# Kernel tuning notes

Hardware: AMD Instinct MI355X
Metric: run time of the kernel (lower is better)

Reference implementation:

```python
import jax, jax.numpy as jnp
import numpy as np

B, L, NB = 8192, 40, 2        # batch, maxlen, behavior features
V, E = 100000, 64             # vocab per table, embed dim per table
NS, ND = 3, 8                 # other sparse feats, dense feats
D = NB * E                    # concatenated behavior embed dim = 128
ALL = D + D + (ND + NS * E)   # info_all dim = 456
NEG_INF = -2.0**32 + 1
BN_EPS = 1e-3                 # keras BatchNormalization default epsilon


def setup_inputs() -> dict:
    key = jax.random.key(0)
    ks = jax.random.split(key, 20)
    inp = {
        "dense_inputs": jax.random.normal(ks[0], (B, ND), jnp.float32),
        "sparse_inputs": jax.random.randint(ks[1], (B, NS), 0, V),
        "seq_inputs": jax.random.randint(ks[2], (B, L, NB), 0, V),
        "item_inputs": jax.random.randint(ks[3], (B, NB), 0, V),
        # embedding tables (random_uniform init in keras)
        "emb_sparse": jax.random.uniform(ks[4], (NS, V, E), jnp.float32, -0.05, 0.05),
        "emb_seq": jax.random.uniform(ks[5], (NB, V, E), jnp.float32, -0.05, 0.05),
        # attention MLP: input 4*D=512 -> 80 -> 40 -> 1
        "att_W1": jax.random.normal(ks[6], (4 * D, 80), jnp.float32) * 0.05,
        "att_b1": jnp.zeros((80,), jnp.float32),
        "att_W2": jax.random.normal(ks[7], (80, 40), jnp.float32) * 0.05,
        "att_b2": jnp.zeros((40,), jnp.float32),
        "att_Wf": jax.random.normal(ks[8], (40, 1), jnp.float32) * 0.05,
        "att_bf": jnp.zeros((1,), jnp.float32),
        # batch norm (inference-mode moving stats)
        "bn_gamma": jnp.ones((ALL,), jnp.float32),
        "bn_beta": jnp.zeros((ALL,), jnp.float32),
        "bn_mean": jnp.zeros((ALL,), jnp.float32),
        "bn_var": jnp.ones((ALL,), jnp.float32),
        # FFN: ALL -> 80 -> 40 -> 1, PReLU alphas per-feature
        "ffn_W1": jax.random.normal(ks[9], (ALL, 80), jnp.float32) * 0.05,
        "ffn_b1": jnp.zeros((80,), jnp.float32),
        "ffn_a1": jnp.full((80,), 0.25, jnp.float32),
        "ffn_W2": jax.random.normal(ks[10], (80, 40), jnp.float32) * 0.05,
        "ffn_b2": jnp.zeros((40,), jnp.float32),
        "ffn_a2": jnp.full((40,), 0.25, jnp.float32),
        "out_W": jax.random.normal(ks[11], (40, 1), jnp.float32) * 0.05,
        "out_b": jnp.zeros((1,), jnp.float32),
    }
    return inp


def prelu(x, alpha):
    return jnp.where(x > 0, x, alpha * x)


def reference(dense_inputs, sparse_inputs, seq_inputs, item_inputs,
              emb_sparse, emb_seq,
              att_W1, att_b1, att_W2, att_b2, att_Wf, att_bf,
              bn_gamma, bn_beta, bn_mean, bn_var,
              ffn_W1, ffn_b1, ffn_a1, ffn_W2, ffn_b2, ffn_a2,
              out_W, out_b):
    mask = (seq_inputs[:, :, 0] != 0)                                   # [B, L]
    # other sparse embeddings + dense features
    other_info = jnp.concatenate(
        [dense_inputs] + [emb_sparse[i][sparse_inputs[:, i]] for i in range(NS)], axis=-1)
    # behavior sequence / candidate item embeddings
    seq_embed = jnp.concatenate([emb_seq[i][seq_inputs[:, :, i]] for i in range(NB)], axis=-1)  # [B,L,D]
    item_embed = jnp.concatenate([emb_seq[i][item_inputs[:, i]] for i in range(NB)], axis=-1)   # [B,D]

    # local activation attention
    q = jnp.broadcast_to(item_embed[:, None, :], seq_embed.shape)       # [B,L,D]
    info = jnp.concatenate([q, seq_embed, q - seq_embed, q * seq_embed], axis=-1)  # [B,L,4D]
    h = jax.nn.sigmoid(info @ att_W1 + att_b1)
    h = jax.nn.sigmoid(h @ att_W2 + att_b2)
    logits = (h @ att_Wf + att_bf)[..., 0]                               # [B,L]
    logits = jnp.where(mask, logits, NEG_INF)
    att = jax.nn.softmax(logits, axis=-1)                                # [B,L]
    user_info = jnp.einsum('bl,bld->bd', att, seq_embed)                 # [B,D]

    info_all = jnp.concatenate([user_info, item_embed, other_info], axis=-1)  # [B,ALL]
    info_all = bn_gamma * (info_all - bn_mean) * jax.lax.rsqrt(bn_var + BN_EPS) + bn_beta
    info_all = prelu(info_all @ ffn_W1 + ffn_b1, ffn_a1)
    info_all = prelu(info_all @ ffn_W2 + ffn_b2, ffn_a2)
    return jax.nn.sigmoid(info_all @ out_W + out_b)                      # [B,1]
```

## Files before the change

### kernel.cpp

```cpp
#include <hip/hip_runtime.h>

#define BB 8192
#define LL 40
#define VV 100000
#define NEG_INF_F (-4294967295.0f)
#define XS 136
#define HS 104
#define XGS 480

typedef __attribute__((ext_vector_type(8))) short short8;
typedef __attribute__((ext_vector_type(4))) float f32x4;

__device__ __forceinline__ unsigned cvt_pk_bf16(float a, float b) {
  unsigned r;
  asm("v_cvt_pk_bf16_f32 %0, %1, %2" : "=v"(r) : "v"(a), "v"(b));
  return r;
}
__device__ __forceinline__ unsigned short f2bf(float f) {
  return (unsigned short)cvt_pk_bf16(f, f);
}
__device__ __forceinline__ float bf2f(unsigned short s) {
  return __uint_as_float(((unsigned)s) << 16);
}
__device__ __forceinline__ float sigm(float z) {
  return __builtin_amdgcn_rcpf(1.f + __expf(-z));
}

__device__ __forceinline__ short8 fuseB(short8 wsd, short8 wd, float4 qa, float4 qb) {
  float qv[8] = {qa.x, qa.y, qa.z, qa.w, qb.x, qb.y, qb.z, qb.w};
  float f[8];
#pragma unroll
  for (int j = 0; j < 8; j++)
    f[j] = bf2f((unsigned short)wsd[j]) + qv[j] * bf2f((unsigned short)wd[j]);
  uint4 o;
  o.x = cvt_pk_bf16(f[0], f[1]);
  o.y = cvt_pk_bf16(f[2], f[3]);
  o.z = cvt_pk_bf16(f[4], f[5]);
  o.w = cvt_pk_bf16(f[6], f[7]);
  return __builtin_bit_cast(short8, o);
}

__global__ void prep_all(const float* __restrict__ W1, float* __restrict__ wqcT,
                         unsigned short* __restrict__ WsdpT,
                         const float* __restrict__ aW2, unsigned short* __restrict__ W2bT,
                         const float* __restrict__ fW2, unsigned short* __restrict__ W2fT,
                         const float* __restrict__ fW1, const float* __restrict__ g,
                         const float* __restrict__ vr, unsigned short* __restrict__ W1fT,
                         const float* __restrict__ fb1, const float* __restrict__ be,
                         const float* __restrict__ mn, float* __restrict__ b1p,
                         const float* __restrict__ embQ, unsigned short* __restrict__ embQb) {
  __shared__ float red[4];
  int bid = blockIdx.x, t = threadIdx.x;
  if (bid < 40) {
    int i = bid * 256 + t;
    int h = i >> 7, k = i & 127;
    float a = W1[k * 80 + h];
    float b = W1[(128 + k) * 80 + h];
    float c = W1[(256 + k) * 80 + h];
    float d = W1[(384 + k) * 80 + h];
    wqcT[h * 132 + k] = a + c;
    WsdpT[h * 256 + k] = f2bf(b - c);
    WsdpT[h * 256 + 128 + k] = f2bf(d);
  } else if (bid < 58) {
    int i = (bid - 40) * 256 + t;
    int n = i / 96, k = i % 96;
    W2bT[i] = (n < 40 && k < 80) ? f2bf(aW2[k * 40 + n]) : (unsigned short)0;
  } else if (bid < 76) {
    int i = (bid - 58) * 256 + t;
    int n = i / 96, k = i % 96;
    W2fT[i] = (n < 40 && k < 80) ? f2bf(fW2[k * 40 + n]) : (unsigned short)0;
  } else if (bid < 226) {
    int i = (bid - 76) * 256 + t;
    int n = i / 480, k = i % 480;
    float v = 0.f;
    if (k < 456) v = fW1[k * 80 + n] * g[k] * rsqrtf(vr[k] + 1e-3f);
    W1fT[i] = f2bf(v);
  } else if (bid < 306) {
    int n = bid - 226;
    float p = 0.f;
    for (int k = t; k < 456; k += 256) {
      float sc = g[k] * rsqrtf(vr[k] + 1e-3f);
      p += (be[k] - mn[k] * sc) * fW1[k * 80 + n];
    }
    for (int off = 32; off; off >>= 1) p += __shfl_xor(p, off, 64);
    if ((t & 63) == 0) red[t >> 6] = p;
    __syncthreads();
    if (t == 0) b1p[n] = fb1[n] + red[0] + red[1] + red[2] + red[3];
  } else {
    const float4* src = (const float4*)embQ;
    uint2* dst = (uint2*)embQb;
    for (int i = (bid - 306) * 256 + t; i < 3200000; i += 2048 * 256) {
      float4 v = src[i];
      uint2 p;
      p.x = cvt_pk_bf16(v.x, v.y);
      p.y = cvt_pk_bf16(v.z, v.w);
      dst[i] = p;
    }
  }
}


__launch_bounds__(256, 8)
__global__ void din_att(const float* __restrict__ dense, const int* __restrict__ sparsei,
                        const int* __restrict__ seqi, const int* __restrict__ itemi,
                        const float* __restrict__ embS, const float* __restrict__ embQ,
                        const unsigned short* __restrict__ embQb,
                        const float* __restrict__ wqcT, const unsigned short* __restrict__ WsdpT,
                        const unsigned short* __restrict__ W2bT,
                        const float* __restrict__ ab1, const float* __restrict__ ab2,
                        const float* __restrict__ aWf, const float* __restrict__ abf,
                        unsigned short* __restrict__ Xg) {
  __shared__ __align__(16) char smem[20352];
  unsigned short* sX  = (unsigned short*)smem;
  unsigned short* sH1 = (unsigned short*)(smem + 10880);
  float* sQ    = (float*)(smem + 19200);
  float* sQCp  = sQ + 128;
  float* sLA   = sQCp + 80;
  float* sMask = sLA + 40;

  const int t = threadIdx.x;
  const int b = blockIdx.x;
  const int wv = t >> 6, ln = t & 63, m16 = ln & 15, quad = ln >> 4;
  unsigned short* xrow = Xg + (size_t)b * XGS;

  if (t < 32) {
    int f = t >> 4, sub = t & 15;
    int idx = itemi[b * 2 + f];
    float4 v = *(const float4*)(embQ + ((size_t)(f * VV + idx)) * 64 + sub * 4);
    *(float4*)(sQ + f * 64 + sub * 4) = v;
    uint2 p;
    p.x = cvt_pk_bf16(v.x, v.y);
    p.y = cvt_pk_bf16(v.z, v.w);
    *(uint2*)(xrow + 128 + f * 64 + sub * 4) = p;
  } else if (t >= 100 && t < 140) {
    sLA[t - 100] = 0.f;
  }
  for (int i = t; i < 320; i += 256) {
    int r = i >> 3, c = i & 7;
    ((unsigned*)sH1)[r * 52 + 40 + c] = 0u;
  }
  __syncthreads();

  uint2 gv[5];
#pragma unroll
  for (int it = 0; it < 5; it++) {
    int i = t + (it << 8);
    int r = i >> 4, sub = i & 15, f = r & 1;
    int idx = seqi[b * 80 + r];
    if (embQb) {
      gv[it] = *(const uint2*)(embQb + ((size_t)(f * VV + idx)) * 64 + sub * 4);
    } else {
      float4 v = *(const float4*)(embQ + ((size_t)(f * VV + idx)) * 64 + sub * 4);
      gv[it].x = cvt_pk_bf16(v.x, v.y);
      gv[it].y = cvt_pk_bf16(v.z, v.w);
    }
  }
  if (t >= 32 && t < 80) {
    int j = t - 32, f = j >> 4, sub = j & 15;
    int idx = sparsei[b * 3 + f];
    float4 v = *(const float4*)(embS + ((size_t)(f * VV + idx)) * 64 + sub * 4);
    uint2 p;
    p.x = cvt_pk_bf16(v.x, v.y);
    p.y = cvt_pk_bf16(v.z, v.w);
    *(uint2*)(xrow + 264 + f * 64 + sub * 4) = p;
  } else if (t >= 80 && t < 88) {
    xrow[256 + (t - 80)] = f2bf(dense[b * 8 + (t - 80)]);
  } else if (t >= 88 && t < 100) {
    ((unsigned*)xrow)[228 + (t - 88)] = 0u;
  }
  if (t < 80) {
    float acc0 = ab1[t], acc1 = 0.f;
    const float* wq = wqcT + t * 132;
    for (int k = 0; k < 128; k += 8) {
      float4 w0 = *(const float4*)(wq + k);
      float4 w1 = *(const float4*)(wq + k + 4);
      float4 q0 = *(const float4*)(sQ + k);
      float4 q1 = *(const float4*)(sQ + k + 4);
      acc0 += q0.x * w0.x + q0.y * w0.y + q0.z * w0.z + q0.w * w0.w;
      acc1 += q1.x * w1.x + q1.y * w1.y + q1.z * w1.z + q1.w * w1.w;
    }
    sQCp[t] = acc0 + acc1;
  }
  short8 Bp[4];
  {
    const unsigned short* br = WsdpT + (size_t)(wv * 16 + m16) * 256 + quad * 8;
#pragma unroll
    for (int kt = 0; kt < 4; kt++) {
      short8 w1 = *(const short8*)(br + kt * 32);
      short8 w2 = *(const short8*)(br + 128 + kt * 32);
      int k0 = quad * 8 + kt * 32;
      Bp[kt] = fuseB(w1, w2, *(const float4*)(sQ + k0), *(const float4*)(sQ + k0 + 4));
    }
  }
#pragma unroll
  for (int it = 0; it < 5; it++) {
    int i = t + (it << 8);
    int r = i >> 4, sub = i & 15, l = r >> 1, f = r & 1;
    *(uint2*)(sX + l * XS + f * 64 + sub * 4) = gv[it];
  }
  if ((t & 31) == 0) {
#pragma unroll
    for (int it = 0; it < 5; it++) {
      int r = (t >> 4) + (it << 4);
      sMask[r >> 1] = (seqi[b * 80 + r] != 0) ? 0.f : NEG_INF_F;
    }
  }
  __syncthreads();

  {
    const int h = wv * 16 + m16;
    const float qc = sQCp[h];
#pragma unroll
    for (int mt = 0; mt < 3; mt++) {
      f32x4 acc = {0.f, 0.f, 0.f, 0.f};
      const unsigned short* ar = sX + (mt * 16 + m16) * XS + quad * 8;
#pragma unroll
      for (int kt = 0; kt < 4; kt++) {
        short8 a = *(const short8*)(ar + kt * 32);
        acc = __builtin_amdgcn_mfma_f32_16x16x32_bf16(a, Bp[kt], acc, 0, 0, 0);
      }
      float s0 = sigm(acc[0] + qc), s1 = sigm(acc[1] + qc);
      float s2 = sigm(acc[2] + qc), s3 = sigm(acc[3] + qc);
      unsigned p01 = cvt_pk_bf16(s0, s1), p23 = cvt_pk_bf16(s2, s3);
      int l0 = mt * 16 + quad * 4;
      if (l0 < 40) {
        sH1[(l0 + 0) * HS + h] = (unsigned short)p01;
        sH1[(l0 + 1) * HS + h] = (unsigned short)(p01 >> 16);
        sH1[(l0 + 2) * HS + h] = (unsigned short)p23;
        sH1[(l0 + 3) * HS + h] = (unsigned short)(p23 >> 16);
      }
    }
    if (wv < 3) {
      const unsigned short* br = WsdpT + (size_t)(64 + m16) * 256 + quad * 8;
      const unsigned short* ar = sX + (wv * 16 + m16) * XS + quad * 8;
      f32x4 acc = {0.f, 0.f, 0.f, 0.f};
#pragma unroll
      for (int kt = 0; kt < 4; kt++) {
        short8 w1 = *(const short8*)(br + kt * 32);
        short8 w2 = *(const short8*)(br + 128 + kt * 32);
        int k0 = quad * 8 + kt * 32;
        short8 bp = fuseB(w1, w2, *(const float4*)(sQ + k0), *(const float4*)(sQ + k0 + 4));
        short8 a = *(const short8*)(ar + kt * 32);
        acc = __builtin_amdgcn_mfma_f32_16x16x32_bf16(a, bp, acc, 0, 0, 0);
      }
      int h4 = 64 + m16;
      float qc4 = sQCp[h4];
      float s0 = sigm(acc[0] + qc4), s1 = sigm(acc[1] + qc4);
      float s2 = sigm(acc[2] + qc4), s3 = sigm(acc[3] + qc4);
      unsigned p01 = cvt_pk_bf16(s0, s1), p23 = cvt_pk_bf16(s2, s3);
      int l0 = wv * 16 + quad * 4;
      if (l0 < 40) {
        sH1[(l0 + 0) * HS + h4] = (unsigned short)p01;
        sH1[(l0 + 1) * HS + h4] = (unsigned short)(p01 >> 16);
        sH1[(l0 + 2) * HS + h4] = (unsigned short)p23;
        sH1[(l0 + 3) * HS + h4] = (unsigned short)(p23 >> 16);
      }
    }
  }
  __syncthreads();

  for (int tile = wv; tile < 9; tile += 4) {
    int mt = tile / 3, nt = tile % 3;
    f32x4 acc = {0.f, 0.f, 0.f, 0.f};
    int arow = mt * 16 + m16;
    if (arow > 39) arow = 39;
    const unsigned short* ar = sH1 + arow * HS + quad * 8;
    const unsigned short* br = W2bT + (nt * 16 + m16) * 96 + quad * 8;
#pragma unroll
    for (int kt = 0; kt < 3; kt++) {
      short8 a = *(const short8*)(ar + kt * 32);
      short8 bb = *(const short8*)(br + kt * 32);
      acc = __builtin_amdgcn_mfma_f32_16x16x32_bf16(a, bb, acc, 0, 0, 0);
    }
    int j = nt * 16 + m16;
    float b2 = (j < 40) ? ab2[j] : 0.f;
    float wf = (j < 40) ? aWf[j] : 0.f;
    float c[4];
#pragma unroll
    for (int r = 0; r < 4; r++) {
      float h2 = sigm(acc[r] + b2);
      c[r] = (j < 40) ? h2 * wf : 0.f;
    }
#pragma unroll
    for (int off = 1; off < 16; off <<= 1) {
#pragma unroll
      for (int r = 0; r < 4; r++) c[r] += __shfl_xor(c[r], off, 64);
    }
    if (m16 == 0) {
#pragma unroll
      for (int r = 0; r < 4; r++) {
        int l = mt * 16 + quad * 4 + r;
        if (l < 40) atomicAdd(&sLA[l], c[r]);
      }
    }
  }
  __syncthreads();

  if (wv < 2) {
    float logit = -3.0e38f;
    if (ln < 40) logit = sLA[ln] + abf[0] + sMask[ln];
    float mx = logit;
    for (int off = 32; off; off >>= 1) mx = fmaxf(mx, __shfl_xor(mx, off, 64));
    float ex = (ln < 40) ? __expf(logit - mx) : 0.f;
    float sm = ex;
    for (int off = 32; off; off >>= 1) sm += __shfl_xor(sm, off, 64);
    float* av = sQCp + wv * 40;
    if (ln < 40) av[ln] = ex * __builtin_amdgcn_rcpf(sm);
    float acc = 0.f;
    for (int l = 0; l < 40; l++) acc += av[l] * bf2f(sX[l * XS + t]);
    xrow[t] = f2bf(acc);
  }
}


__launch_bounds__(256, 2)
__global__ void din_ffn(const unsigned short* __restrict__ Xg,
                        const unsigned short* __restrict__ W1fT, const float* __restrict__ b1p,
                        const float* __restrict__ fa1,
                        const unsigned short* __restrict__ W2fT, const float* __restrict__ fb2,
                        const float* __restrict__ fa2,
                        const float* __restrict__ oW, const float* __restrict__ ob,
                        float* __restrict__ out) {
  __shared__ __align__(16) unsigned short sXB[16 * 488];
  __shared__ __align__(16) unsigned short sH1B[16 * HS];
  __shared__ float sH2B[16 * 41];
  const int t = threadIdx.x, blk = blockIdx.x;
  const int wv = t >> 6, ln = t & 63, m16 = ln & 15, quad = ln >> 4;

  short8 Bf[15];
  {
    const unsigned short* br = W1fT + (size_t)(wv * 16 + m16) * 480 + quad * 8;
#pragma unroll
    for (int kt = 0; kt < 15; kt++) Bf[kt] = *(const short8*)(br + kt * 32);
  }

  for (int i = t; i < 960; i += 256) {
    int r = i / 60, c = i % 60;
    *(uint4*)(sXB + r * 488 + c * 8) =
        *(const uint4*)(Xg + (size_t)(blk * 16 + r) * XGS + c * 8);
  }
  if (t < 128) {
    int r = t >> 3, c = t & 7;
    ((unsigned*)sH1B)[r * 52 + 40 + c] = 0u;
  }
  __syncthreads();

  {
    int h = wv * 16 + m16;
    f32x4 acc = {0.f, 0.f, 0.f, 0.f};
    const unsigned short* ar = sXB + m16 * 488 + quad * 8;
#pragma unroll
    for (int kt = 0; kt < 15; kt++) {
      short8 a = *(const short8*)(ar + kt * 32);
      acc = __builtin_amdgcn_mfma_f32_16x16x32_bf16(a, Bf[kt], acc, 0, 0, 0);
    }
    float b1v = b1p[h], a1v = fa1[h];
    float z0 = acc[0] + b1v, z1 = acc[1] + b1v, z2 = acc[2] + b1v, z3 = acc[3] + b1v;
    z0 = z0 > 0.f ? z0 : a1v * z0;
    z1 = z1 > 0.f ? z1 : a1v * z1;
    z2 = z2 > 0.f ? z2 : a1v * z2;
    z3 = z3 > 0.f ? z3 : a1v * z3;
    unsigned p01 = cvt_pk_bf16(z0, z1), p23 = cvt_pk_bf16(z2, z3);
    int l0 = quad * 4;
    sH1B[(l0 + 0) * HS + h] = (unsigned short)p01;
    sH1B[(l0 + 1) * HS + h] = (unsigned short)(p01 >> 16);
    sH1B[(l0 + 2) * HS + h] = (unsigned short)p23;
    sH1B[(l0 + 3) * HS + h] = (unsigned short)(p23 >> 16);
    if (wv == 0) {
      short8 B4[15];
      const unsigned short* br = W1fT + (size_t)(64 + m16) * 480 + quad * 8;
#pragma unroll
      for (int kt = 0; kt < 15; kt++) B4[kt] = *(const short8*)(br + kt * 32);
      f32x4 acc4 = {0.f, 0.f, 0.f, 0.f};
#pragma unroll
      for (int kt = 0; kt < 15; kt++) {
        short8 a = *(const short8*)(ar + kt * 32);
        acc4 = __builtin_amdgcn_mfma_f32_16x16x32_bf16(a, B4[kt], acc4, 0, 0, 0);
      }
      int h4 = 64 + m16;
      float b1v4 = b1p[h4], a1v4 = fa1[h4];
      float y0 = acc4[0] + b1v4, y1 = acc4[1] + b1v4, y2 = acc4[2] + b1v4, y3 = acc4[3] + b1v4;
      y0 = y0 > 0.f ? y0 : a1v4 * y0;
      y1 = y1 > 0.f ? y1 : a1v4 * y1;
      y2 = y2 > 0.f ? y2 : a1v4 * y2;
      y3 = y3 > 0.f ? y3 : a1v4 * y3;
      unsigned q01 = cvt_pk_bf16(y0, y1), q23 = cvt_pk_bf16(y2, y3);
      sH1B[(l0 + 0) * HS + h4] = (unsigned short)q01;
      sH1B[(l0 + 1) * HS + h4] = (unsigned short)(q01 >> 16);
      sH1B[(l0 + 2) * HS + h4] = (unsigned short)q23;
      sH1B[(l0 + 3) * HS + h4] = (unsigned short)(q23 >> 16);
    }
  }
  __syncthreads();

  if (wv < 3) {
    f32x4 acc = {0.f, 0.f, 0.f, 0.f};
    const unsigned short* ar = sH1B + m16 * HS + quad * 8;
    const unsigned short* br = W2fT + (wv * 16 + m16) * 96 + quad * 8;
#pragma unroll
    for (int kt = 0; kt < 3; kt++) {
      short8 a = *(const short8*)(ar + kt * 32);
      short8 bb = *(const short8*)(br + kt * 32);
      acc = __builtin_amdgcn_mfma_f32_16x16x32_bf16(a, bb, acc, 0, 0, 0);
    }
    int j = wv * 16 + m16;
    if (j < 40) {
      float b2 = fb2[j], a2 = fa2[j];
#pragma unroll
      for (int r = 0; r < 4; r++) {
        int l = quad * 4 + r;
        float z = acc[r] + b2;
        sH2B[l * 41 + j] = z > 0.f ? z : a2 * z;
      }
    }
  }
  __syncthreads();

  if (t < 16) {
    float acc = ob[0];
    for (int j = 0; j < 40; j++) acc += sH2B[t * 41 + j] * oW[j];
    out[blk * 16 + t] = sigm(acc);
  }
}


extern "C" void kernel_launch(void* const* d_in, const int* in_sizes, int n_in,
                              void* d_out, int out_size, void* d_ws, size_t ws_size,
                              hipStream_t stream) {
  const float* dense  = (const float*)d_in[0];
  const int*   sparsei = (const int*)d_in[1];
  const int*   seqi   = (const int*)d_in[2];
  const int*   itemi  = (const int*)d_in[3];
  const float* embS   = (const float*)d_in[4];
  const float* embQ   = (const float*)d_in[5];
  const float* aW1    = (const float*)d_in[6];
  const float* ab1    = (const float*)d_in[7];
  const float* aW2    = (const float*)d_in[8];
  const float* ab2    = (const float*)d_in[9];
  const float* aWf    = (const float*)d_in[10];
  const float* abf    = (const float*)d_in[11];
  const float* bng    = (const float*)d_in[12];
  const float* bnb    = (const float*)d_in[13];
  const float* bnm    = (const float*)d_in[14];
  const float* bnv    = (const float*)d_in[15];
  const float* fW1    = (const float*)d_in[16];
  const float* fb1    = (const float*)d_in[17];
  const float* fa1    = (const float*)d_in[18];
  const float* fW2    = (const float*)d_in[19];
  const float* fb2    = (const float*)d_in[20];
  const float* fa2    = (const float*)d_in[21];
  const float* oW     = (const float*)d_in[22];
  const float* ob     = (const float*)d_in[23];
  float* out = (float*)d_out;

  float* ws = (float*)d_ws;
  float* wqcT = ws;
  float* b1p  = ws + 10560;
  unsigned short* WsdpT = (unsigned short*)(ws + 10640);
  unsigned short* W2bT  = (unsigned short*)(ws + 20880);
  unsigned short* W2fT  = (unsigned short*)(ws + 23184);
  unsigned short* W1fT  = (unsigned short*)(ws + 25488);
  unsigned short* Xg    = (unsigned short*)(ws + 44688);

  size_t base = 44688ull * 4 + 8192ull * 480 * 2;
  size_t need = base + 12800000ull * 2;
  unsigned short* embQb = (ws_size >= need)
      ? (unsigned short*)((char*)d_ws + base) : (unsigned short*)0;

  int prep_grid = embQb ? 2354 : 306;
  prep_all<<<prep_grid, 256, 0, stream>>>(aW1, wqcT, WsdpT, aW2, W2bT, fW2, W2fT,
                                          fW1, bng, bnv, W1fT, fb1, bnb, bnm, b1p,
                                          embQ, embQb);
  din_att<<<BB, 256, 0, stream>>>(dense, sparsei, seqi, itemi, embS, embQ, embQb,
                                  wqcT, WsdpT, W2bT, ab1, ab2, aWf, abf, Xg);
  din_ffn<<<512, 256, 0, stream>>>(Xg, W1fT, b1p, fa1, W2fT, fb2, fa2, oW, ob, out);
}
```

Measured before the change: 335.5 us.

## Drop full bf16 table conversion; widen FFN block to five waves

Removes the prep pass that converted the entire 2x100000x64 fp32 sequence embedding table to bf16 on every call, and has the attention kernel gather fp32 rows directly and convert them in registers. This avoids reading about 51 MB and writing about 26 MB per call, at the cost of doubling the bytes fetched per gathered row. The FFN kernel is launched with 320 threads so a fifth wave computes the last 16 hidden units instead of wave 0 doing two tiles serially, and launch bounds and load strides are adjusted to match.

```diff
diff --git a/kernel.cpp b/kernel.cpp
--- a/kernel.cpp
+++ b/kernel.cpp
@@ -47,8 +47,7 @@
                          const float* __restrict__ fW1, const float* __restrict__ g,
                          const float* __restrict__ vr, unsigned short* __restrict__ W1fT,
                          const float* __restrict__ fb1, const float* __restrict__ be,
-                         const float* __restrict__ mn, float* __restrict__ b1p,
-                         const float* __restrict__ embQ, unsigned short* __restrict__ embQb) {
+                         const float* __restrict__ mn, float* __restrict__ b1p) {
   __shared__ float red[4];
   int bid = blockIdx.x, t = threadIdx.x;
   if (bid < 40) {
@@ -75,7 +74,7 @@
     float v = 0.f;
     if (k < 456) v = fW1[k * 80 + n] * g[k] * rsqrtf(vr[k] + 1e-3f);
     W1fT[i] = f2bf(v);
-  } else if (bid < 306) {
+  } else {
     int n = bid - 226;
     float p = 0.f;
     for (int k = t; k < 456; k += 256) {
@@ -86,16 +85,6 @@
     if ((t & 63) == 0) red[t >> 6] = p;
     __syncthreads();
     if (t == 0) b1p[n] = fb1[n] + red[0] + red[1] + red[2] + red[3];
-  } else {
-    const float4* src = (const float4*)embQ;
-    uint2* dst = (uint2*)embQb;
-    for (int i = (bid - 306) * 256 + t; i < 3200000; i += 2048 * 256) {
-      float4 v = src[i];
-      uint2 p;
-      p.x = cvt_pk_bf16(v.x, v.y);
-      p.y = cvt_pk_bf16(v.z, v.w);
-      dst[i] = p;
-    }
   }
 }
 
@@ -104,7 +93,6 @@
 __global__ void din_att(const float* __restrict__ dense, const int* __restrict__ sparsei,
                         const int* __restrict__ seqi, const int* __restrict__ itemi,
                         const float* __restrict__ embS, const float* __restrict__ embQ,
-                        const unsigned short* __restrict__ embQb,
                         const float* __restrict__ wqcT, const unsigned short* __restrict__ WsdpT,
                         const unsigned short* __restrict__ W2bT,
                         const float* __restrict__ ab1, const float* __restrict__ ab2,
@@ -147,13 +135,9 @@
     int i = t + (it << 8);
     int r = i >> 4, sub = i & 15, f = r & 1;
     int idx = seqi[b * 80 + r];
-    if (embQb) {
-      gv[it] = *(const uint2*)(embQb + ((size_t)(f * VV + idx)) * 64 + sub * 4);
-    } else {
-      float4 v = *(const float4*)(embQ + ((size_t)(f * VV + idx)) * 64 + sub * 4);
-      gv[it].x = cvt_pk_bf16(v.x, v.y);
-      gv[it].y = cvt_pk_bf16(v.z, v.w);
-    }
+    float4 v = *(const float4*)(embQ + ((size_t)(f * VV + idx)) * 64 + sub * 4);
+    gv[it].x = cvt_pk_bf16(v.x, v.y);
+    gv[it].y = cvt_pk_bf16(v.z, v.w);
   }
   if (t >= 32 && t < 80) {
     int j = t - 32, f = j >> 4, sub = j & 15;
@@ -313,7 +297,7 @@
 }
 
 
-__launch_bounds__(256, 2)
+__launch_bounds__(320, 2)
 __global__ void din_ffn(const unsigned short* __restrict__ Xg,
                         const unsigned short* __restrict__ W1fT, const float* __restrict__ b1p,
                         const float* __restrict__ fa1,
@@ -334,7 +318,7 @@
     for (int kt = 0; kt < 15; kt++) Bf[kt] = *(const short8*)(br + kt * 32);
   }
 
-  for (int i = t; i < 960; i += 256) {
+  for (int i = t; i < 960; i += 320) {
     int r = i / 60, c = i % 60;
     *(uint4*)(sXB + r * 488 + c * 8) =
         *(const uint4*)(Xg + (size_t)(blk * 16 + r) * XGS + c * 8);
@@ -366,30 +350,6 @@
     sH1B[(l0 + 1) * HS + h] = (unsigned short)(p01 >> 16);
     sH1B[(l0 + 2) * HS + h] = (unsigned short)p23;
     sH1B[(l0 + 3) * HS + h] = (unsigned short)(p23 >> 16);
-    if (wv == 0) {
-      short8 B4[15];
-      const unsigned short* br = W1fT + (size_t)(64 + m16) * 480 + quad * 8;
-#pragma unroll
-      for (int kt = 0; kt < 15; kt++) B4[kt] = *(const short8*)(br + kt * 32);
-      f32x4 acc4 = {0.f, 0.f, 0.f, 0.f};
-#pragma unroll
-      for (int kt = 0; kt < 15; kt++) {
-        short8 a = *(const short8*)(ar + kt * 32);
-        acc4 = __builtin_amdgcn_mfma_f32_16x16x32_bf16(a, B4[kt], acc4, 0, 0, 0);
-      }
-      int h4 = 64 + m16;
-      float b1v4 = b1p[h4], a1v4 = fa1[h4];
-      float y0 = acc4[0] + b1v4, y1 = acc4[1] + b1v4, y2 = acc4[2] + b1v4, y3 = acc4[3] + b1v4;
-      y0 = y0 > 0.f ? y0 : a1v4 * y0;
-      y1 = y1 > 0.f ? y1 : a1v4 * y1;
-      y2 = y2 > 0.f ? y2 : a1v4 * y2;
-      y3 = y3 > 0.f ? y3 : a1v4 * y3;
-      unsigned q01 = cvt_pk_bf16(y0, y1), q23 = cvt_pk_bf16(y2, y3);
-      sH1B[(l0 + 0) * HS + h4] = (unsigned short)q01;
-      sH1B[(l0 + 1) * HS + h4] = (unsigned short)(q01 >> 16);
-      sH1B[(l0 + 2) * HS + h4] = (unsigned short)q23;
-      sH1B[(l0 + 3) * HS + h4] = (unsigned short)(q23 >> 16);
-    }
   }
   __syncthreads();
 
@@ -462,16 +422,9 @@
   unsigned short* W1fT  = (unsigned short*)(ws + 25488);
   unsigned short* Xg    = (unsigned short*)(ws + 44688);
 
-  size_t base = 44688ull * 4 + 8192ull * 480 * 2;
-  size_t need = base + 12800000ull * 2;
-  unsigned short* embQb = (ws_size >= need)
-      ? (unsigned short*)((char*)d_ws + base) : (unsigned short*)0;
-
-  int prep_grid = embQb ? 2354 : 306;
-  prep_all<<<prep_grid, 256, 0, stream>>>(aW1, wqcT, WsdpT, aW2, W2bT, fW2, W2fT,
-                                          fW1, bng, bnv, W1fT, fb1, bnb, bnm, b1p,
-                                          embQ, embQb);
-  din_att<<<BB, 256, 0, stream>>>(dense, sparsei, seqi, itemi, embS, embQ, embQb,
+  prep_all<<<306, 256, 0, stream>>>(aW1, wqcT, WsdpT, aW2, W2bT, fW2, W2fT,
+                                    fW1, bng, bnv, W1fT, fb1, bnb, bnm, b1p);
+  din_att<<<BB, 256, 0, stream>>>(dense, sparsei, seqi, itemi, embS, embQ,
                                   wqcT, WsdpT, W2bT, ab1, ab2, aWf, abf, Xg);
-  din_ffn<<<512, 256, 0, stream>>>(Xg, W1fT, b1p, fa1, W2fT, fb2, fa2, oW, ob, out);
-}
+  din_ffn<<<512, 320, 0, stream>>>(Xg, W1fT, b1p, fa1, W2fT, fb2, fa2, oW, ob, out);
+}
```

Result: faster. 316.5 us (-5.7%).
